# Kernel tuning notes

Hardware: AMD Instinct MI355X
Metric: run time of the kernel (lower is better)

The kernel has to match this reference:

```python
import jax, jax.numpy as jnp
import numpy as np
from jax import lax

EPS = 0.1
MAX_ITER = 50
LOG_EPS = 1e-8


def setup_inputs() -> dict:
    key = jax.random.key(0)
    k1, k2, k3 = jax.random.split(key, 3)
    N, P1, P2 = 8, 2048, 2048
    C = jax.random.uniform(k1, (N, P1, P2), dtype=jnp.float32)
    mu = jax.random.uniform(k2, (N, P1), dtype=jnp.float32)
    nu = jax.random.uniform(k3, (N, P2), dtype=jnp.float32)
    # empirical measures: normalize to probability simplices
    mu = mu / jnp.sum(mu, axis=-1, keepdims=True)
    nu = nu / jnp.sum(nu, axis=-1, keepdims=True)
    return {"C": C, "mu": mu, "nu": nu}


def reference(C, mu, nu):
    """Log-domain Sinkhorn. Returns (cost, pi, C) like the torch module
    (reduction='none'). Fixed MAX_ITER iterations (the torch early-exit
    err.item() check is a host sync; fixed-count scan computes the same
    update math)."""
    log_mu = jnp.log(mu + LOG_EPS)  # (N, P1)
    log_nu = jnp.log(nu + LOG_EPS)  # (N, P2)

    def M(u, v):
        # (-C_ij + u_i + v_j) / eps  -> (N, P1, P2)
        return (-C + u[..., :, None] + v[..., None, :]) / EPS

    def step(carry, _):
        u, v = carry
        u = EPS * (log_mu - jax.nn.logsumexp(M(u, v), axis=-1)) + u
        v = EPS * (log_nu - jax.nn.logsumexp(M(u, v), axis=-2)) + v
        return (u, v), None

    u0 = jnp.zeros_like(mu)
    v0 = jnp.zeros_like(nu)
    (u, v), _ = lax.scan(step, (u0, v0), None, length=MAX_ITER)

    pi = jnp.exp(M(u, v))                 # transport plan (N, P1, P2)
    cost = jnp.sum(pi * C, axis=(-2, -1))  # (N,)
    return cost, pi, C
```

## Files before the change

### kernel.cpp

```cpp
#include <hip/hip_runtime.h>
#include <hip/hip_fp16.h>

#define N_B 8
#define P 2048
#define NP (N_B * P)
#define EPS 0.1f
#define IEPS 10.0f
#define LOG_EPS 1e-8f
#define MAX_ITER 50

typedef float f4 __attribute__((ext_vector_type(4)));

__global__ __launch_bounds__(256) void k_init(const float* __restrict__ nu,
                                              float* __restrict__ s0) {
    int idx = blockIdx.x * 256 + threadIdx.x;
    s0[idx] = nu[idx] + LOG_EPS;
}

__global__ __launch_bounds__(256) void k_build(const float* __restrict__ C,
                                               __half* __restrict__ K) {
    size_t idx = ((size_t)blockIdx.x * 256 + threadIdx.x) * 4;
    float4 c = *(const float4*)(C + idx);
    __half2 h01 = __floats2half2_rn(expf(-IEPS * c.x), expf(-IEPS * c.y));
    __half2 h23 = __floats2half2_rn(expf(-IEPS * c.z), expf(-IEPS * c.w));
    *(__half2*)(K + idx)     = h01;
    *(__half2*)(K + idx + 2) = h23;
}

__global__ __launch_bounds__(256) void k_build2(const float* __restrict__ C,
                                                __half* __restrict__ K,
                                                __half* __restrict__ KT) {
    __shared__ __half sh[64][72];
    int b = blockIdx.x;
    const int tj = b & 31; b >>= 5;
    const int ti = b & 31; b >>= 5;
    const int n  = b;
    const int tid = threadIdx.x;
    const int lr = tid >> 4;
    const int lc = (tid & 15) * 4;
    #pragma unroll
    for (int e = 0; e < 4; ++e) {
        const int r = e * 16 + lr;
        const size_t off = ((size_t)(n * P + ti * 64 + r)) * P + tj * 64 + lc;
        f4 c4 = *(const f4*)(C + off);
        __half h0 = __float2half(expf(-IEPS * c4.x));
        __half h1 = __float2half(expf(-IEPS * c4.y));
        __half h2 = __float2half(expf(-IEPS * c4.z));
        __half h3 = __float2half(expf(-IEPS * c4.w));
        *(__half2*)(K + off)     = __halves2half2(h0, h1);
        *(__half2*)(K + off + 2) = __halves2half2(h2, h3);
        sh[r][lc] = h0; sh[r][lc + 1] = h1; sh[r][lc + 2] = h2; sh[r][lc + 3] = h3;
    }
    __syncthreads();
    #pragma unroll
    for (int e = 0; e < 4; ++e) {
        const int r = e * 16 + lr;
        const size_t off = ((size_t)(n * P + tj * 64 + r)) * P + ti * 64 + lc;
        *(__half2*)(KT + off)     = __halves2half2(sh[lc][r],     sh[lc + 1][r]);
        *(__half2*)(KT + off + 2) = __halves2half2(sh[lc + 2][r], sh[lc + 3][r]);
    }
}

template <int PASS>
__global__ __launch_bounds__(256) void k_pass(const __half* __restrict__ Km,
                                              const float* __restrict__ mu,
                                              const float* __restrict__ nu,
                                              const float* __restrict__ vin,
                                              float* __restrict__ vout) {
    const int tid  = threadIdx.x;
    const int n    = blockIdx.x >> 8;
    const int r0   = (blockIdx.x & 255) * 8;
    const int wave = tid >> 6, lane = tid & 63;
    const float* vn  = vin + n * P;
    const float* nun = nu  + n * P;

    f4 areg[8];
    #pragma unroll
    for (int q = 0; q < 4; ++q) {
        const int j = q * 512 + lane * 8;
        f4 sv0 = *(const f4*)(vn + j);
        f4 sv1 = *(const f4*)(vn + j + 4);
        if (PASS == 0) {
            f4 nv0 = *(const f4*)(nun + j);
            f4 nv1 = *(const f4*)(nun + j + 4);
            f4 a0, a1;
            a0.x = (nv0.x + LOG_EPS) / sv0.x;
            a0.y = (nv0.y + LOG_EPS) / sv0.y;
            a0.z = (nv0.z + LOG_EPS) / sv0.z;
            a0.w = (nv0.w + LOG_EPS) / sv0.w;
            a1.x = (nv1.x + LOG_EPS) / sv1.x;
            a1.y = (nv1.y + LOG_EPS) / sv1.y;
            a1.z = (nv1.z + LOG_EPS) / sv1.z;
            a1.w = (nv1.w + LOG_EPS) / sv1.w;
            areg[2 * q] = a0; areg[2 * q + 1] = a1;
        } else {
            areg[2 * q] = sv0; areg[2 * q + 1] = sv1;
        }
    }

    #pragma unroll
    for (int rp = 0; rp < 2; ++rp) {
        const int i = r0 + wave + rp * 4;
        const size_t rowoff = (size_t)(n * P + i) * P;
        float sa = 0.f, sb = 0.f;
        #pragma unroll
        for (int q = 0; q < 4; ++q) {
            const int j = q * 512 + lane * 8;
            f4 kv = *(const f4*)(Km + rowoff + j);
            const __half2* kh = (const __half2*)&kv;
            float2 f0 = __half22float2(kh[0]);
            float2 f1 = __half22float2(kh[1]);
            float2 f2 = __half22float2(kh[2]);
            float2 f3 = __half22float2(kh[3]);
            f4 a0 = areg[2 * q], a1 = areg[2 * q + 1];
            sa += f0.x * a0.x + f0.y * a0.y + f1.x * a0.z + f1.y * a0.w;
            sb += f2.x * a1.x + f2.y * a1.y + f3.x * a1.z + f3.y * a1.w;
        }
        float sum = sa + sb;
        #pragma unroll
        for (int off = 32; off > 0; off >>= 1) sum += __shfl_down(sum, off, 64);
        if (lane == 0) {
            if (PASS == 0) vout[n * P + i] = (mu[n * P + i] + LOG_EPS) / sum;
            else           vout[n * P + i] = sum;
        }
    }
}

template <bool USEK>
__global__ __launch_bounds__(256) void k_row(const __half* __restrict__ K,
                                             const float* __restrict__ C,
                                             const float* __restrict__ mu,
                                             const float* __restrict__ nu,
                                             const float* __restrict__ sA,
                                             float* __restrict__ sB,
                                             float* __restrict__ w) {
    __shared__ float a_sh[P];
    const int tid = threadIdx.x;
    if (blockIdx.x < NP / 256) sB[blockIdx.x * 256 + tid] = 0.f;

    const int n  = blockIdx.x >> 8;
    const int r0 = (blockIdx.x & 255) * 8;
    const float* sAn = sA + n * P;
    const float* nun = nu + n * P;
    for (int j = tid; j < P; j += 256)
        a_sh[j] = (nun[j] + LOG_EPS) / sAn[j];
    __syncthreads();

    const int wave = tid >> 6, lane = tid & 63;
    for (int rr = wave; rr < 8; rr += 4) {
        const int i = r0 + rr;
        const size_t rowoff = (size_t)(n * P + i) * P;
        float sum = 0.f;
        #pragma unroll
        for (int jj = 0; jj < P; jj += 256) {
            const int j = jj + lane * 4;
            float4 av = *(const float4*)&a_sh[j];
            float k0, k1, k2, k3;
            if (USEK) {
                const __half2* kp = (const __half2*)(K + rowoff + j);
                float2 f01 = __half22float2(kp[0]);
                float2 f23 = __half22float2(kp[1]);
                k0 = f01.x; k1 = f01.y; k2 = f23.x; k3 = f23.y;
            } else {
                float4 c4 = *(const float4*)(C + rowoff + j);
                k0 = expf(-IEPS * c4.x); k1 = expf(-IEPS * c4.y);
                k2 = expf(-IEPS * c4.z); k3 = expf(-IEPS * c4.w);
            }
            sum += k0 * av.x + k1 * av.y + k2 * av.z + k3 * av.w;
        }
        #pragma unroll
        for (int off = 32; off > 0; off >>= 1) sum += __shfl_down(sum, off, 64);
        if (lane == 0) w[n * P + i] = (mu[n * P + i] + LOG_EPS) / sum;
    }
}

template <bool USEK>
__global__ __launch_bounds__(256) void k_col(const __half* __restrict__ K,
                                             const float* __restrict__ C,
                                             const float* __restrict__ w,
                                             float* __restrict__ sB) {
    const int RPB = 64;
    int b = blockIdx.x;
    const int rc = b & 31; b >>= 5;
    const int jt = b & 3;  b >>= 2;
    const int n  = b;
    const int j  = jt * 512 + threadIdx.x * 2;
    const int i0 = rc * RPB;
    const float* wn = w + n * P;
    float s0 = 0.f, s1 = 0.f;
    if (USEK) {
        const __half2* kp = (const __half2*)(K + ((size_t)n * P + i0) * P + j);
        #pragma unroll 4
        for (int i = 0; i < RPB; ++i) {
            const float wi = wn[i0 + i];
            float2 kv = __half22float2(*kp);
            s0 += wi * kv.x; s1 += wi * kv.y;
            kp += P / 2;
        }
    } else {
        const float* cp = C + ((size_t)n * P + i0) * P + j;
        #pragma unroll 2
        for (int i = 0; i < RPB; ++i) {
            const float wi = wn[i0 + i];
            s0 += wi * expf(-IEPS * cp[0]);
            s1 += wi * expf(-IEPS * cp[1]);
            cp += P;
        }
    }
    atomicAdd(&sB[n * P + j],     s0);
    atomicAdd(&sB[n * P + j + 1], s1);
}

__global__ __launch_bounds__(256) void k_a(const float* __restrict__ nu,
                                           const float* __restrict__ s,
                                           float* __restrict__ a) {
    int idx = blockIdx.x * 256 + threadIdx.x;
    a[idx] = (nu[idx] + LOG_EPS) / s[idx];
}

__global__ __launch_bounds__(256) void k_final(const float* __restrict__ C,
                                               const float* __restrict__ a,
                                               const float* __restrict__ w,
                                               float* __restrict__ part,
                                               float* __restrict__ out) {
    const int g   = blockIdx.x;
    const int n   = g >> 11;
    const int tid = threadIdx.x;
    const float wi = w[g];
    const size_t rowoff = (size_t)g * P;
    const float* Crow = C + rowoff;
    const float* an   = a + (size_t)n * P;
    float* pi_out = out + N_B + rowoff;
    float* c_out  = out + N_B + (size_t)NP * P + rowoff;
    float cost = 0.f;
    #pragma unroll
    for (int jj = 0; jj < P; jj += 1024) {
        const int j = jj + tid * 4;
        f4 c4 = *(const f4*)(Crow + j);
        f4 a4 = *(const f4*)(an + j);
        f4 p;
        p.x = wi * a4.x * expf(-IEPS * c4.x);
        p.y = wi * a4.y * expf(-IEPS * c4.y);
        p.z = wi * a4.z * expf(-IEPS * c4.z);
        p.w = wi * a4.w * expf(-IEPS * c4.w);
        __builtin_nontemporal_store(p,  (f4*)(pi_out + j));
        __builtin_nontemporal_store(c4, (f4*)(c_out + j));
        cost += p.x * c4.x + p.y * c4.y + p.z * c4.z + p.w * c4.w;
    }
    const int wave = tid >> 6, lane = tid & 63;
    #pragma unroll
    for (int off = 32; off > 0; off >>= 1) cost += __shfl_down(cost, off, 64);
    __shared__ float red[4];
    if (lane == 0) red[wave] = cost;
    __syncthreads();
    if (tid == 0) part[g] = red[0] + red[1] + red[2] + red[3];
}

__global__ __launch_bounds__(256) void k_reduce(const float* __restrict__ part,
                                                float* __restrict__ out) {
    const int n = blockIdx.x, tid = threadIdx.x;
    float s = 0.f;
    for (int b = tid; b < P; b += 256) s += part[(size_t)n * P + b];
    const int wave = tid >> 6, lane = tid & 63;
    #pragma unroll
    for (int off = 32; off > 0; off >>= 1) s += __shfl_down(s, off, 64);
    __shared__ float red[4];
    if (lane == 0) red[wave] = s;
    __syncthreads();
    if (tid == 0) out[n] = red[0] + red[1] + red[2] + red[3];
}

extern "C" void kernel_launch(void* const* d_in, const int* in_sizes, int n_in,
                              void* d_out, int out_size, void* d_ws, size_t ws_size,
                              hipStream_t stream) {
    const float* C  = (const float*)d_in[0];
    const float* mu = (const float*)d_in[1];
    const float* nu = (const float*)d_in[2];
    float* out = (float*)d_out;

    float* s0 = (float*)d_ws;
    float* s1 = s0 + NP;
    float* w  = s1 + NP;
    __half* K  = (__half*)(w + NP);
    __half* KT = K + (size_t)NP * P;
    const size_t base   = 3ull * NP * sizeof(float);
    const size_t needK  = base + (size_t)NP * P * sizeof(__half);
    const size_t needKT = base + 2ull * (size_t)NP * P * sizeof(__half);
    const int tier = (ws_size >= needKT) ? 2 : (ws_size >= needK) ? 1 : 0;

    k_init<<<NP / 256, 256, 0, stream>>>(nu, s0);

    if (tier == 2) {
        k_build2<<<N_B * 32 * 32, 256, 0, stream>>>(C, K, KT);
        for (int t = 0; t < MAX_ITER; ++t) {
            float* sA = (t & 1) ? s1 : s0;
            float* sB = (t & 1) ? s0 : s1;
            k_pass<0><<<NP / 8, 256, 0, stream>>>(K,  mu, nu, sA, w);
            k_pass<1><<<NP / 8, 256, 0, stream>>>(KT, mu, nu, w,  sB);
        }
    } else if (tier == 1) {
        k_build<<<((size_t)NP * P) / 1024, 256, 0, stream>>>(C, K);
        for (int t = 0; t < MAX_ITER; ++t) {
            float* sA = (t & 1) ? s1 : s0;
            float* sB = (t & 1) ? s0 : s1;
            k_row<true><<<NP / 8, 256, 0, stream>>>(K, C, mu, nu, sA, sB, w);
            k_col<true><<<8 * 4 * 32, 256, 0, stream>>>(K, C, w, sB);
        }
    } else {
        for (int t = 0; t < MAX_ITER; ++t) {
            float* sA = (t & 1) ? s1 : s0;
            float* sB = (t & 1) ? s0 : s1;
            k_row<false><<<NP / 8, 256, 0, stream>>>(K, C, mu, nu, sA, sB, w);
            k_col<false><<<8 * 4 * 32, 256, 0, stream>>>(K, C, w, sB);
        }
    }

    float* aBuf = s1;
    float* part = s0;
    k_a<<<NP / 256, 256, 0, stream>>>(nu, s0, aBuf);
    k_final<<<NP, 256, 0, stream>>>(C, aBuf, w, part, out);
    k_reduce<<<N_B, 256, 0, stream>>>(part, out);
}
```

Before: 1.628 ms.

## Fuse row and column Sinkhorn passes via LDS-staged K tile, drop transposed KT

Each iteration now reads K once: a block loads 16 rows into shared memory, computes the row scaling w, then reuses the staged rows to produce per-block column partial sums, which a small reduction kernel combines into the new column scaling. This removes the transposed K copy and its second full read per iteration. In exchange it adds a partials buffer write/read and uses 64 KB of LDS per block, limiting occupancy.

New measurement: 1.342 ms. 1.21x faster.

```diff
diff --git a/kernel.cpp b/kernel.cpp
--- a/kernel.cpp
+++ b/kernel.cpp
@@ -8,11 +8,18 @@
 #define IEPS 10.0f
 #define LOG_EPS 1e-8f
 #define MAX_ITER 50
+#define RPB 16
+#define NRB (P / RPB)
 
 typedef float f4 __attribute__((ext_vector_type(4)));
 
-__global__ __launch_bounds__(256) void k_init(const float* __restrict__ nu,
-                                              float* __restrict__ s0) {
+__global__ __launch_bounds__(256) void k_init_one(float* __restrict__ a) {
+    int idx = blockIdx.x * 256 + threadIdx.x;
+    a[idx] = 1.0f;
+}
+
+__global__ __launch_bounds__(256) void k_init_nu(const float* __restrict__ nu,
+                                                 float* __restrict__ s0) {
     int idx = blockIdx.x * 256 + threadIdx.x;
     s0[idx] = nu[idx] + LOG_EPS;
 }
@@ -27,86 +34,38 @@
     *(__half2*)(K + idx + 2) = h23;
 }
 
-__global__ __launch_bounds__(256) void k_build2(const float* __restrict__ C,
-                                                __half* __restrict__ K,
-                                                __half* __restrict__ KT) {
-    __shared__ __half sh[64][72];
-    int b = blockIdx.x;
-    const int tj = b & 31; b >>= 5;
-    const int ti = b & 31; b >>= 5;
-    const int n  = b;
-    const int tid = threadIdx.x;
-    const int lr = tid >> 4;
-    const int lc = (tid & 15) * 4;
-    #pragma unroll
-    for (int e = 0; e < 4; ++e) {
-        const int r = e * 16 + lr;
-        const size_t off = ((size_t)(n * P + ti * 64 + r)) * P + tj * 64 + lc;
-        f4 c4 = *(const f4*)(C + off);
-        __half h0 = __float2half(expf(-IEPS * c4.x));
-        __half h1 = __float2half(expf(-IEPS * c4.y));
-        __half h2 = __float2half(expf(-IEPS * c4.z));
-        __half h3 = __float2half(expf(-IEPS * c4.w));
-        *(__half2*)(K + off)     = __halves2half2(h0, h1);
-        *(__half2*)(K + off + 2) = __halves2half2(h2, h3);
-        sh[r][lc] = h0; sh[r][lc + 1] = h1; sh[r][lc + 2] = h2; sh[r][lc + 3] = h3;
-    }
-    __syncthreads();
-    #pragma unroll
-    for (int e = 0; e < 4; ++e) {
-        const int r = e * 16 + lr;
-        const size_t off = ((size_t)(n * P + tj * 64 + r)) * P + ti * 64 + lc;
-        *(__half2*)(KT + off)     = __halves2half2(sh[lc][r],     sh[lc + 1][r]);
-        *(__half2*)(KT + off + 2) = __halves2half2(sh[lc + 2][r], sh[lc + 3][r]);
-    }
-}
-
-template <int PASS>
-__global__ __launch_bounds__(256) void k_pass(const __half* __restrict__ Km,
-                                              const float* __restrict__ mu,
-                                              const float* __restrict__ nu,
-                                              const float* __restrict__ vin,
-                                              float* __restrict__ vout) {
-    const int tid  = threadIdx.x;
-    const int n    = blockIdx.x >> 8;
-    const int r0   = (blockIdx.x & 255) * 8;
-    const int wave = tid >> 6, lane = tid & 63;
-    const float* vn  = vin + n * P;
-    const float* nun = nu  + n * P;
+__global__ __launch_bounds__(256) void k_fused(const __half* __restrict__ Km,
+                                               const float* __restrict__ mu,
+                                               const float* __restrict__ a,
+                                               float* __restrict__ w,
+                                               float* __restrict__ part) {
+    __shared__ __half ksh[RPB * P];
+    __shared__ float  w_sh[RPB];
+    const int tid = threadIdx.x, wave = tid >> 6, lane = tid & 63;
+    const int n  = blockIdx.x >> 7;
+    const int rb = blockIdx.x & 127;
+    const int r0 = rb * RPB;
+    const float* an = a + n * P;
 
     f4 areg[8];
     #pragma unroll
     for (int q = 0; q < 4; ++q) {
         const int j = q * 512 + lane * 8;
-        f4 sv0 = *(const f4*)(vn + j);
-        f4 sv1 = *(const f4*)(vn + j + 4);
-        if (PASS == 0) {
-            f4 nv0 = *(const f4*)(nun + j);
-            f4 nv1 = *(const f4*)(nun + j + 4);
-            f4 a0, a1;
-            a0.x = (nv0.x + LOG_EPS) / sv0.x;
-            a0.y = (nv0.y + LOG_EPS) / sv0.y;
-            a0.z = (nv0.z + LOG_EPS) / sv0.z;
-            a0.w = (nv0.w + LOG_EPS) / sv0.w;
-            a1.x = (nv1.x + LOG_EPS) / sv1.x;
-            a1.y = (nv1.y + LOG_EPS) / sv1.y;
-            a1.z = (nv1.z + LOG_EPS) / sv1.z;
-            a1.w = (nv1.w + LOG_EPS) / sv1.w;
-            areg[2 * q] = a0; areg[2 * q + 1] = a1;
-        } else {
-            areg[2 * q] = sv0; areg[2 * q + 1] = sv1;
-        }
-    }
-
-    #pragma unroll
-    for (int rp = 0; rp < 2; ++rp) {
-        const int i = r0 + wave + rp * 4;
+        areg[2 * q]     = *(const f4*)(an + j);
+        areg[2 * q + 1] = *(const f4*)(an + j + 4);
+    }
+
+    #pragma unroll
+    for (int rr = 0; rr < 4; ++rr) {
+        const int r = wave * 4 + rr;
+        const int i = r0 + r;
         const size_t rowoff = (size_t)(n * P + i) * P;
         float sa = 0.f, sb = 0.f;
         #pragma unroll
         for (int q = 0; q < 4; ++q) {
             const int j = q * 512 + lane * 8;
             f4 kv = *(const f4*)(Km + rowoff + j);
+            *(f4*)(ksh + r * P + j) = kv;
             const __half2* kh = (const __half2*)&kv;
             float2 f0 = __half22float2(kh[0]);
             float2 f1 = __half22float2(kh[1]);
@@ -120,9 +79,58 @@
         #pragma unroll
         for (int off = 32; off > 0; off >>= 1) sum += __shfl_down(sum, off, 64);
         if (lane == 0) {
-            if (PASS == 0) vout[n * P + i] = (mu[n * P + i] + LOG_EPS) / sum;
-            else           vout[n * P + i] = sum;
-        }
+            float wi = (mu[n * P + i] + LOG_EPS) / sum;
+            w_sh[r] = wi;
+            w[n * P + i] = wi;
+        }
+    }
+    __syncthreads();
+
+    const int j0 = tid * 8;
+    float s[8];
+    #pragma unroll
+    for (int q = 0; q < 8; ++q) s[q] = 0.f;
+    #pragma unroll 4
+    for (int r = 0; r < RPB; ++r) {
+        const float wr = w_sh[r];
+        f4 kv = *(const f4*)(ksh + r * P + j0);
+        const __half2* kh = (const __half2*)&kv;
+        float2 f0 = __half22float2(kh[0]);
+        float2 f1 = __half22float2(kh[1]);
+        float2 f2 = __half22float2(kh[2]);
+        float2 f3 = __half22float2(kh[3]);
+        s[0] += wr * f0.x; s[1] += wr * f0.y;
+        s[2] += wr * f1.x; s[3] += wr * f1.y;
+        s[4] += wr * f2.x; s[5] += wr * f2.y;
+        s[6] += wr * f3.x; s[7] += wr * f3.y;
+    }
+    float* pp = part + ((size_t)(n * NRB + rb)) * P + j0;
+    f4 o0, o1;
+    o0.x = s[0]; o0.y = s[1]; o0.z = s[2]; o0.w = s[3];
+    o1.x = s[4]; o1.y = s[5]; o1.z = s[6]; o1.w = s[7];
+    *(f4*)(pp)     = o0;
+    *(f4*)(pp + 4) = o1;
+}
+
+__global__ __launch_bounds__(256) void k_red(const float* __restrict__ part,
+                                             const float* __restrict__ nu,
+                                             float* __restrict__ aOut) {
+    const int n  = blockIdx.x >> 5;
+    const int jb = blockIdx.x & 31;
+    const int tid = threadIdx.x;
+    const int rq = tid >> 6, jj = tid & 63;
+    const int j = jb * 64 + jj;
+    const float* pp = part + (size_t)n * NRB * P + (size_t)(rq * 32) * P + j;
+    float s = 0.f;
+    #pragma unroll 8
+    for (int r = 0; r < 32; ++r) s += pp[(size_t)r * P];
+    __shared__ float red[4][64];
+    red[rq][jj] = s;
+    __syncthreads();
+    if (rq == 0) {
+        const float t = red[0][jj] + red[1][jj] + red[2][jj] + red[3][jj];
+        const int idx = n * P + j;
+        aOut[idx] = (nu[idx] + LOG_EPS) / t;
     }
 }
 
@@ -179,19 +187,19 @@
                                              const float* __restrict__ C,
                                              const float* __restrict__ w,
                                              float* __restrict__ sB) {
-    const int RPB = 64;
+    const int CRPB = 64;
     int b = blockIdx.x;
     const int rc = b & 31; b >>= 5;
     const int jt = b & 3;  b >>= 2;
     const int n  = b;
     const int j  = jt * 512 + threadIdx.x * 2;
-    const int i0 = rc * RPB;
+    const int i0 = rc * CRPB;
     const float* wn = w + n * P;
     float s0 = 0.f, s1 = 0.f;
     if (USEK) {
         const __half2* kp = (const __half2*)(K + ((size_t)n * P + i0) * P + j);
         #pragma unroll 4
-        for (int i = 0; i < RPB; ++i) {
+        for (int i = 0; i < CRPB; ++i) {
             const float wi = wn[i0 + i];
             float2 kv = __half22float2(*kp);
             s0 += wi * kv.x; s1 += wi * kv.y;
@@ -200,7 +208,7 @@
     } else {
         const float* cp = C + ((size_t)n * P + i0) * P + j;
         #pragma unroll 2
-        for (int i = 0; i < RPB; ++i) {
+        for (int i = 0; i < CRPB; ++i) {
             const float wi = wn[i0 + i];
             s0 += wi * expf(-IEPS * cp[0]);
             s1 += wi * expf(-IEPS * cp[1]);
@@ -221,7 +229,7 @@
 __global__ __launch_bounds__(256) void k_final(const float* __restrict__ C,
                                                const float* __restrict__ a,
                                                const float* __restrict__ w,
-                                               float* __restrict__ part,
+                                               float* __restrict__ cpart,
                                                float* __restrict__ out) {
     const int g   = blockIdx.x;
     const int n   = g >> 11;
@@ -253,14 +261,14 @@
     __shared__ float red[4];
     if (lane == 0) red[wave] = cost;
     __syncthreads();
-    if (tid == 0) part[g] = red[0] + red[1] + red[2] + red[3];
-}
-
-__global__ __launch_bounds__(256) void k_reduce(const float* __restrict__ part,
+    if (tid == 0) cpart[g] = red[0] + red[1] + red[2] + red[3];
+}
+
+__global__ __launch_bounds__(256) void k_reduce(const float* __restrict__ cpart,
                                                 float* __restrict__ out) {
     const int n = blockIdx.x, tid = threadIdx.x;
     float s = 0.f;
-    for (int b = tid; b < P; b += 256) s += part[(size_t)n * P + b];
+    for (int b = tid; b < P; b += 256) s += cpart[(size_t)n * P + b];
     const int wave = tid >> 6, lane = tid & 63;
     #pragma unroll
     for (int off = 32; off > 0; off >>= 1) s += __shfl_down(s, off, 64);
@@ -278,46 +286,49 @@
     const float* nu = (const float*)d_in[2];
     float* out = (float*)d_out;
 
-    float* s0 = (float*)d_ws;
-    float* s1 = s0 + NP;
-    float* w  = s1 + NP;
-    __half* K  = (__half*)(w + NP);
-    __half* KT = K + (size_t)NP * P;
-    const size_t base   = 3ull * NP * sizeof(float);
-    const size_t needK  = base + (size_t)NP * P * sizeof(__half);
-    const size_t needKT = base + 2ull * (size_t)NP * P * sizeof(__half);
-    const int tier = (ws_size >= needKT) ? 2 : (ws_size >= needK) ? 1 : 0;
-
-    k_init<<<NP / 256, 256, 0, stream>>>(nu, s0);
+    float* v0 = (float*)d_ws;
+    float* v1 = v0 + NP;
+    float* v2 = v1 + NP;
+    float* part8 = v2 + NP;
+    __half* K = (__half*)(part8 + (size_t)N_B * NRB * P);
+    const size_t base     = 3ull * NP * sizeof(float);
+    const size_t needK    = base + (size_t)NP * P * sizeof(__half);
+    const size_t needFuse = base + (size_t)N_B * NRB * P * sizeof(float)
+                                 + (size_t)NP * P * sizeof(__half);
+    __half* K1 = (__half*)(v2 + NP);
+    const int tier = (ws_size >= needFuse) ? 2 : (ws_size >= needK) ? 1 : 0;
 
     if (tier == 2) {
-        k_build2<<<N_B * 32 * 32, 256, 0, stream>>>(C, K, KT);
-        for (int t = 0; t < MAX_ITER; ++t) {
-            float* sA = (t & 1) ? s1 : s0;
-            float* sB = (t & 1) ? s0 : s1;
-            k_pass<0><<<NP / 8, 256, 0, stream>>>(K,  mu, nu, sA, w);
-            k_pass<1><<<NP / 8, 256, 0, stream>>>(KT, mu, nu, w,  sB);
-        }
-    } else if (tier == 1) {
+        k_init_one<<<NP / 256, 256, 0, stream>>>(v0);
         k_build<<<((size_t)NP * P) / 1024, 256, 0, stream>>>(C, K);
         for (int t = 0; t < MAX_ITER; ++t) {
-            float* sA = (t & 1) ? s1 : s0;
-            float* sB = (t & 1) ? s0 : s1;
-            k_row<true><<<NP / 8, 256, 0, stream>>>(K, C, mu, nu, sA, sB, w);
-            k_col<true><<<8 * 4 * 32, 256, 0, stream>>>(K, C, w, sB);
-        }
+            k_fused<<<N_B * NRB, 256, 0, stream>>>(K, mu, v0, v1, part8);
+            k_red<<<N_B * 32, 256, 0, stream>>>(part8, nu, v0);
+        }
+        k_final<<<NP, 256, 0, stream>>>(C, v0, v1, v2, out);
+        k_reduce<<<N_B, 256, 0, stream>>>(v2, out);
+    } else if (tier == 1) {
+        k_init_nu<<<NP / 256, 256, 0, stream>>>(nu, v0);
+        k_build<<<((size_t)NP * P) / 1024, 256, 0, stream>>>(C, K1);
+        for (int t = 0; t < MAX_ITER; ++t) {
+            float* sA = (t & 1) ? v1 : v0;
+            float* sB = (t & 1) ? v0 : v1;
+            k_row<true><<<NP / 8, 256, 0, stream>>>(K1, C, mu, nu, sA, sB, v2);
+            k_col<true><<<8 * 4 * 32, 256, 0, stream>>>(K1, C, v2, sB);
+        }
+        k_a<<<NP / 256, 256, 0, stream>>>(nu, v0, v1);
+        k_final<<<NP, 256, 0, stream>>>(C, v1, v2, v0, out);
+        k_reduce<<<N_B, 256, 0, stream>>>(v0, out);
     } else {
+        k_init_nu<<<NP / 256, 256, 0, stream>>>(nu, v0);
         for (int t = 0; t < MAX_ITER; ++t) {
-            float* sA = (t & 1) ? s1 : s0;
-            float* sB = (t & 1) ? s0 : s1;
-            k_row<false><<<NP / 8, 256, 0, stream>>>(K, C, mu, nu, sA, sB, w);
-            k_col<false><<<8 * 4 * 32, 256, 0, stream>>>(K, C, w, sB);
-        }
-    }
-
-    float* aBuf = s1;
-    float* part = s0;
-    k_a<<<NP / 256, 256, 0, stream>>>(nu, s0, aBuf);
-    k_final<<<NP, 256, 0, stream>>>(C, aBuf, w, part, out);
-    k_reduce<<<N_B, 256, 0, stream>>>(part, out);
-}
+            float* sA = (t & 1) ? v1 : v0;
+            float* sB = (t & 1) ? v0 : v1;
+            k_row<false><<<NP / 8, 256, 0, stream>>>(nullptr, C, mu, nu, sA, sB, v2);
+            k_col<false><<<8 * 4 * 32, 256, 0, stream>>>(nullptr, C, v2, sB);
+        }
+        k_a<<<NP / 256, 256, 0, stream>>>(nu, v0, v1);
+        k_final<<<NP, 256, 0, stream>>>(C, v1, v2, v0, out);
+        k_reduce<<<N_B, 256, 0, stream>>>(v0, out);
+    }
+}
```
